# Optimization experiments

Measured on AMD Instinct MI355X. Metric: run time of the kernel, lower is better.

The kernel has to match this reference:

```python
import jax, jax.numpy as jnp
import numpy as np

B, S, D, H = 4, 2048, 512, 8


def _ln(x, g, b, eps=1e-5):
    m = x.mean(-1, keepdims=True)
    v = ((x - m) ** 2).mean(-1, keepdims=True)
    return (x - m) / jnp.sqrt(v + eps) * g + b


def setup_inputs() -> dict:
    key = jax.random.key(0)
    ks = iter(jax.random.split(key, 32))
    n = lambda shape, s=0.02: jax.random.normal(next(ks), shape, jnp.float32) * s
    z = lambda *shape: jnp.zeros(shape, jnp.float32)
    o = lambda *shape: jnp.ones(shape, jnp.float32)
    return {
        "x": jax.random.normal(next(ks), (B, S, D), jnp.float32),
        "x_prev": jax.random.normal(next(ks), (B, S, D), jnp.float32),
        "mu": jnp.float32(0.5),
        "in_proj_w": n((3 * D, D)), "in_proj_b": z(3 * D),
        "out_w": n((D, D)), "out_b": z(D),
        "ln1_g": o(D), "ln1_b": z(D),
        "time_mod": jnp.full((D,), 0.5, jnp.float32),
        "sm_ln_g": o(D), "sm_ln_b": z(D),
        "wr_w": n((D, D)), "wr_b": z(D),
        "wv_w": n((D, D)), "wv_b": z(D),
        "sc_ln_g": o(D), "sc_ln_b": z(D),
        "ln2_g": o(D), "ln2_b": z(D),
        "w1": n((4 * D, D)), "b1": z(4 * D),
        "w2": n((D, 4 * D)), "b2": z(D),
        "ln3_g": o(D), "ln3_b": z(D),
    }


def reference(x, x_prev, mu, in_proj_w, in_proj_b, out_w, out_b, ln1_g, ln1_b,
              time_mod, sm_ln_g, sm_ln_b, wr_w, wr_b, wv_w, wv_b,
              sc_ln_g, sc_ln_b, ln2_g, ln2_b, w1, b1, w2, b2, ln3_g, ln3_b):
    Bs, Sl, Dm = x.shape
    hd = Dm // H
    # Shift (x_prev is not None)
    shifted = mu * x + (1.0 - mu) * x_prev
    # Multihead self-attention (eval mode; dropout = identity)
    qkv = shifted @ in_proj_w.T + in_proj_b
    q, k, v = jnp.split(qkv, 3, axis=-1)
    q = q.reshape(Bs, Sl, H, hd)
    k = k.reshape(Bs, Sl, H, hd)
    v = v.reshape(Bs, Sl, H, hd)
    scores = jnp.einsum('bqhd,bkhd->bhqk', q, k) / jnp.sqrt(jnp.float32(hd))
    attn = jax.nn.softmax(scores, axis=-1)
    ao = jnp.einsum('bhqk,bkhd->bqhd', attn, v).reshape(Bs, Sl, Dm)
    ao = ao @ out_w.T + out_b
    x1 = _ln(shifted + ao, ln1_g, ln1_b)
    # SequenceMergingSeq with C = V = W = x1: sequential decayed running sums
    def step(carry, xt):  # xt: [B, D]
        a, b = carry
        decay = jax.nn.sigmoid(xt * time_mod)
        e = jnp.exp(xt)
        a = decay.mean(-1, keepdims=True) * a + e.sum(-1, keepdims=True)
        b = decay * b + e * xt
        return (a, b), b / (a + 1e-8)
    a0 = jnp.zeros((Bs, 1), x1.dtype)
    b0 = jnp.zeros((Bs, Dm), x1.dtype)
    _, outs = jax.lax.scan(step, (a0, b0), jnp.swapaxes(x1, 0, 1))  # [S,B,D]
    merged = _ln(jnp.swapaxes(outs, 0, 1), sm_ln_g, sm_ln_b)
    # StateCoupling
    coupled = _ln(jax.nn.sigmoid(merged @ wr_w.T + wr_b) * (merged @ wv_w.T + wv_b),
                  sc_ln_g, sc_ln_b)
    x2 = _ln(x1 + coupled, ln2_g, ln2_b)
    # FFN
    ffn = jax.nn.relu(x2 @ w1.T + b1) @ w2.T + b2
    return _ln(x2 + ffn, ln3_g, ln3_b)
```

## Files before the change

### kernel.cpp

```cpp
#include <hip/hip_runtime.h>
#include <math.h>

#define D_MODEL 512
#define SEQ     2048
#define BATCH   4
#define NH      8
#define HD      64
#define CHUNK   32
#define NCHUNK  64
#define M_TOK   (BATCH*SEQ)

typedef __attribute__((ext_vector_type(8))) short bhalf8;
typedef __attribute__((ext_vector_type(4))) float f32x4;

__device__ __forceinline__ float sigmoidf_(float x){ return 1.f/(1.f+expf(-x)); }

__device__ __forceinline__ unsigned short f2b(float f){
  unsigned u = __float_as_uint(f);
  u += 0x7FFFu + ((u>>16)&1u);
  return (unsigned short)(u>>16);
}
__device__ __forceinline__ float b2f(unsigned short h){
  return __uint_as_float(((unsigned)h)<<16);
}
__device__ __forceinline__ float blo(unsigned v){ return __uint_as_float(v<<16); }
__device__ __forceinline__ float bhi(unsigned v){ return __uint_as_float(v & 0xFFFF0000u); }
__device__ __forceinline__ unsigned bpack(float a, float b){
  return (unsigned)f2b(a) | ((unsigned)f2b(b)<<16);
}

__device__ __forceinline__ void gll16(const void* g, void* l){
  __builtin_amdgcn_global_load_lds(
      (const __attribute__((address_space(1))) unsigned int*)g,
      (__attribute__((address_space(3))) unsigned int*)l, 16, 0, 0);
}

__device__ __forceinline__ float exp2_hw(float x){
  float r;
  asm volatile("v_exp_f32 %0, %1" : "=v"(r) : "v"(x));
  return r;
}

__device__ __forceinline__ void block_sum2(float& a, float& b, float* lds){
  #pragma unroll
  for (int o=32;o>0;o>>=1){ a += __shfl_xor(a,o); b += __shfl_xor(b,o); }
  int w = threadIdx.x>>6, l = threadIdx.x&63;
  if (l==0){ lds[2*w]=a; lds[2*w+1]=b; }
  __syncthreads();
  float ta=0.f, tb=0.f; int nw = blockDim.x>>6;
  for (int i=0;i<nw;++i){ ta+=lds[2*i]; tb+=lds[2*i+1]; }
  a=ta; b=tb;
  __syncthreads();
}

__global__ void cvtshift_k(const float* __restrict__ s0,const float* __restrict__ s1,
                           const float* __restrict__ s2,const float* __restrict__ s3,
                           const float* __restrict__ s4,const float* __restrict__ s5,
                           unsigned short* __restrict__ d0,unsigned short* __restrict__ d1,
                           unsigned short* __restrict__ d2,unsigned short* __restrict__ d3,
                           unsigned short* __restrict__ d4,unsigned short* __restrict__ d5,
                           const float* __restrict__ x, const float* __restrict__ xp,
                           const float* __restrict__ mu,
                           unsigned short* __restrict__ ob){
  int t = blockIdx.x*blockDim.x + threadIdx.x;
  if (t < 917504){
    int j = t;
    const float* s; unsigned short* d;
    if (j < 196608){ s=s0; d=d0; }
    else if ((j-=196608) < 65536){ s=s1; d=d1; }
    else if ((j-=65536)  < 65536){ s=s2; d=d2; }
    else if ((j-=65536)  < 65536){ s=s3; d=d3; }
    else if ((j-=65536)  < 262144){ s=s4; d=d4; }
    else { j-=262144; s=s5; d=d5; }
    float4 v = ((const float4*)s)[j];
    uint2 p; p.x = bpack(v.x, v.y); p.y = bpack(v.z, v.w);
    ((uint2*)d)[j] = p;
  } else {
    int i = t - 917504;
    float m = mu[0];
    float4 a = ((const float4*)x)[i], p = ((const float4*)xp)[i];
    float4 r;
    r.x = m*a.x + (1.f-m)*p.x; r.y = m*a.y + (1.f-m)*p.y;
    r.z = m*a.z + (1.f-m)*p.z; r.w = m*a.w + (1.f-m)*p.w;
    uint2 q; q.x = bpack(r.x, r.y); q.y = bpack(r.z, r.w);
    ((uint2*)ob)[i] = q;
  }
}

template<int ACT, int OUTB>
__global__ __launch_bounds__(256) void mgemm_k(const unsigned short* __restrict__ A,
    const unsigned short* __restrict__ W, const float* __restrict__ bias,
    float* __restrict__ Yf, unsigned short* __restrict__ Yb, int Nd, int K){
  __shared__ unsigned short As[128*64];
  __shared__ unsigned short Bs[128*64];
  const int tid = threadIdx.x;
  const int w = tid>>6, lane = tid&63;
  const int l15 = lane&15, l4 = lane>>4;
  const int wr = w>>1, wc = w&1;
  const int nwg = gridDim.x*gridDim.y;
  const int orig = blockIdx.y*gridDim.x + blockIdx.x;
  const int swz = (orig&7)*(nwg>>3) + (orig>>3);
  const int bn = swz % gridDim.x;
  const int bm = swz / gridDim.x;

  const size_t Kb = (size_t)K*2;
  const int srow  = lane>>3;
  const int sbyte = ((lane&7)*16) ^ (srow<<4);
  const char* Ag = (const char*)A + (size_t)(bm*128)*Kb + sbyte;
  const char* Wg = (const char*)W + (size_t)(bn*128)*Kb + sbyte;

  f32x4 acc[4][4];
  const f32x4 z = {0.f,0.f,0.f,0.f};
  #pragma unroll
  for (int i=0;i<4;++i)
    #pragma unroll
    for (int j=0;j<4;++j) acc[i][j] = z;

  const int KT = K/64;
  for (int kt=0; kt<KT; ++kt){
    if (kt) __syncthreads();
    const size_t kOff = (size_t)kt*128;
    #pragma unroll
    for (int i=0;i<4;++i){
      int c = w*4 + i;
      int r = c*8 + srow;
      gll16(Ag + (size_t)r*Kb + kOff, (char*)As + c*1024);
      gll16(Wg + (size_t)r*Kb + kOff, (char*)Bs + c*1024);
    }
    __syncthreads();

    bhalf8 af[4][2], bf_[4][2];
    #pragma unroll
    for (int fr=0; fr<4; ++fr){
      int row = wr*64 + fr*16 + l15;
      #pragma unroll
      for (int ks=0; ks<2; ++ks){
        int byo = (l4*16 + ks*64) ^ ((row&7)<<4);
        af[fr][ks] = *(const bhalf8*)((const char*)As + row*128 + byo);
      }
    }
    #pragma unroll
    for (int fc=0; fc<4; ++fc){
      int row = wc*64 + fc*16 + l15;
      #pragma unroll
      for (int ks=0; ks<2; ++ks){
        int byo = (l4*16 + ks*64) ^ ((row&7)<<4);
        bf_[fc][ks] = *(const bhalf8*)((const char*)Bs + row*128 + byo);
      }
    }
    #pragma unroll
    for (int ks=0; ks<2; ++ks)
      #pragma unroll
      for (int fr=0; fr<4; ++fr)
        #pragma unroll
        for (int fc=0; fc<4; ++fc)
          acc[fr][fc] = __builtin_amdgcn_mfma_f32_16x16x32_bf16(af[fr][ks], bf_[fc][ks], acc[fr][fc], 0, 0, 0);
  }

  const int rowBase = bm*128 + wr*64;
  const int colBase = bn*128 + wc*64;
  #pragma unroll
  for (int fc=0; fc<4; ++fc){
    int col = colBase + fc*16 + l15;
    float bv = bias[col];
    #pragma unroll
    for (int fr=0; fr<4; ++fr){
      #pragma unroll
      for (int j=0; j<4; ++j){
        int row = rowBase + fr*16 + l4*4 + j;
        float v = acc[fr][fc][j] + bv;
        if (ACT) v = fmaxf(v, 0.f);
        if (OUTB) Yb[(size_t)row*Nd + col] = f2b(v);
        else      Yf[(size_t)row*Nd + col] = v;
      }
    }
  }
}

template<int ACT, int FUSE2, int SPLITK>
__global__ __launch_bounds__(256) void mgemm64_k(const unsigned short* __restrict__ A,
    const unsigned short* __restrict__ W0, const unsigned short* __restrict__ W1v,
    const float* __restrict__ bias0, const float* __restrict__ bias1,
    unsigned short* __restrict__ Yb0, unsigned short* __restrict__ Yb1,
    int Nd, int K){
  __shared__ unsigned short As[128*64];
  __shared__ unsigned short Bs[64*64];
  const int tid = threadIdx.x;
  const int w = tid>>6, lane = tid&63;
  const int l15 = lane&15, l4 = lane>>4;
  const int wr = w>>1, wc = w&1;
  const int nwg = gridDim.x*gridDim.y;
  const int orig = blockIdx.y*gridDim.x + blockIdx.x;
  const int swz = (orig&7)*(nwg>>3) + (orig>>3);
  int bn = swz % gridDim.x;
  const int bm = swz / gridDim.x;
  const unsigned short* W = W0;
  const float* bias = bias0;
  unsigned short* Yb = Yb0;
  int half = 0;
  if (FUSE2 && bn >= 8){ W = W1v; bias = bias1; Yb = Yb1; bn -= 8; }
  if (SPLITK && bn >= 8){ half = 1; Yb = Yb1; bn -= 8; }

  const int Ksr = SPLITK ? (K>>1) : K;
  const size_t Kb = (size_t)K*2;
  const size_t hOff = (size_t)half * Ksr * 2;
  const int srow  = lane>>3;
  const int sbyte = ((lane&7)*16) ^ (srow<<4);
  const char* Ag = (const char*)A + (size_t)(bm*128)*Kb + hOff + sbyte;
  const char* Wg = (const char*)W + (size_t)(bn*64)*Kb + hOff + sbyte;

  f32x4 acc[4][2];
  const f32x4 z = {0.f,0.f,0.f,0.f};
  #pragma unroll
  for (int i=0;i<4;++i)
    #pragma unroll
    for (int j=0;j<2;++j) acc[i][j] = z;

  const int KT = Ksr/64;
  for (int kt=0; kt<KT; ++kt){
    if (kt) __syncthreads();
    const size_t kOff = (size_t)kt*128;
    #pragma unroll
    for (int i=0;i<4;++i){
      int c = w*4 + i;
      int r = c*8 + srow;
      gll16(Ag + (size_t)r*Kb + kOff, (char*)As + c*1024);
    }
    #pragma unroll
    for (int i=0;i<2;++i){
      int c = w*2 + i;
      int r = c*8 + srow;
      gll16(Wg + (size_t)r*Kb + kOff, (char*)Bs + c*1024);
    }
    __syncthreads();

    bhalf8 af[4][2], bf_[2][2];
    #pragma unroll
    for (int fr=0; fr<4; ++fr){
      int row = wr*64 + fr*16 + l15;
      #pragma unroll
      for (int ks=0; ks<2; ++ks){
        int byo = (l4*16 + ks*64) ^ ((row&7)<<4);
        af[fr][ks] = *(const bhalf8*)((const char*)As + row*128 + byo);
      }
    }
    #pragma unroll
    for (int fc=0; fc<2; ++fc){
      int row = wc*32 + fc*16 + l15;
      #pragma unroll
      for (int ks=0; ks<2; ++ks){
        int byo = (l4*16 + ks*64) ^ ((row&7)<<4);
        bf_[fc][ks] = *(const bhalf8*)((const char*)Bs + row*128 + byo);
      }
    }
    #pragma unroll
    for (int ks=0; ks<2; ++ks)
      #pragma unroll
      for (int fr=0; fr<4; ++fr)
        #pragma unroll
        for (int fc=0; fc<2; ++fc)
          acc[fr][fc] = __builtin_amdgcn_mfma_f32_16x16x32_bf16(af[fr][ks], bf_[fc][ks], acc[fr][fc], 0, 0, 0);
  }

  const int rowBase = bm*128 + wr*64;
  const int colBase = bn*64 + wc*32;
  #pragma unroll
  for (int fc=0; fc<2; ++fc){
    int col = colBase + fc*16 + l15;
    float bv = (SPLITK && half) ? 0.f : bias[col];
    #pragma unroll
    for (int fr=0; fr<4; ++fr){
      #pragma unroll
      for (int j=0; j<4; ++j){
        int row = rowBase + fr*16 + l4*4 + j;
        float v = acc[fr][fc][j] + bv;
        if (ACT) v = fmaxf(v, 0.f);
        Yb[(size_t)row*Nd + col] = f2b(v);
      }
    }
  }
}

__global__ __launch_bounds__(512, 4) void fattn_k(const unsigned short* __restrict__ qkv,
                                                  unsigned short* __restrict__ ao){
  __shared__ unsigned short Ks[2][64*64];
  __shared__ unsigned short Vt[2][64*64];
  __shared__ unsigned short Ps[128*64];
  const int nwg = gridDim.x*gridDim.y*gridDim.z;
  const int orig = (blockIdx.z*gridDim.y + blockIdx.y)*gridDim.x + blockIdx.x;
  const int swz = (orig&7)*(nwg>>3) + (orig>>3);
  const int qt = swz % gridDim.x;
  const int rem = swz / gridDim.x;
  const int h = rem % gridDim.y;
  const int b = rem / gridDim.y;
  const int tid = threadIdx.x, w = tid>>6, lane = tid&63;
  const int l15 = lane&15, l4 = lane>>4;
  const size_t rowB = 3072;
  const char* base = (const char*)qkv + (size_t)b*SEQ*rowB;
  const char* Kg = base + 1024 + h*128;
  const char* Vg = base + 2048 + h*128;
  const float C2 = 0.18033688f;

  bhalf8 qf[2];
  {
    const char* qrow = base + (size_t)(qt*128 + w*16 + l15)*rowB + h*128;
    qf[0] = *(const bhalf8*)(qrow + l4*16);
    qf[1] = *(const bhalf8*)(qrow + l4*16 + 64);
  }
  bhalf8 v1;
  {
    short o = (l15==0) ? (short)0x3F80 : (short)0;
    v1 = (bhalf8){o,o,o,o,o,o,o,o};
  }

  const f32x4 z = {0.f,0.f,0.f,0.f};
  f32x4 oa[4], ol = z;
  #pragma unroll
  for (int i=0;i<4;++i) oa[i] = z;
  float mj = -INFINITY;

  const int srow  = lane>>3;
  const int sbyte = ((lane&7)*16) ^ (srow<<4);
  const int vd = lane;
  const int vsel = (vd>>3)&1;

  unsigned short vload[8];
  {
    int r = w*8 + srow;
    gll16(Kg + (size_t)r*rowB + sbyte, (char*)Ks[0] + w*1024);
  }
  #pragma unroll
  for (int i=0;i<8;++i)
    vload[i] = *(const unsigned short*)(Vg + (size_t)(w*8 + i)*rowB + vd*2);

  int cur = 0;
  for (int kt=0; kt<SEQ/64; ++kt){
    #pragma unroll
    for (int i=0;i<2;++i){
      int p = i ^ vsel;
      unsigned lo = (unsigned)vload[p*4+0] | ((unsigned)vload[p*4+1]<<16);
      unsigned hi = (unsigned)vload[p*4+2] | ((unsigned)vload[p*4+3]<<16);
      uint2 pk; pk.x = lo; pk.y = hi;
      int byo = (w*16 + p*8) ^ ((vd&7)<<4);
      *(uint2*)((char*)Vt[cur] + vd*128 + byo) = pk;
    }
    __syncthreads();

    if (kt+1 < SEQ/64){
      int r = w*8 + srow;
      gll16(Kg + (size_t)((kt+1)*64 + r)*rowB + sbyte, (char*)Ks[cur^1] + w*1024);
      #pragma unroll
      for (int i=0;i<8;++i)
        vload[i] = *(const unsigned short*)(Vg + (size_t)((kt+1)*64 + w*8 + i)*rowB + vd*2);
    }

    bhalf8 kf[4][2];
    #pragma unroll
    for (int fc=0; fc<4; ++fc){
      int kr = fc*16 + l15;
      #pragma unroll
      for (int ks=0; ks<2; ++ks){
        int byo = (l4*16 + ks*64) ^ ((kr&7)<<4);
        kf[fc][ks] = *(const bhalf8*)((const char*)Ks[cur] + kr*128 + byo);
      }
    }
    f32x4 s[4];
    #pragma unroll
    for (int i=0;i<4;++i) s[i] = z;
    __builtin_amdgcn_s_setprio(1);
    #pragma unroll
    for (int ks=0; ks<2; ++ks)
      #pragma unroll
      for (int fc=0; fc<4; ++fc)
        s[fc] = __builtin_amdgcn_mfma_f32_16x16x32_bf16(kf[fc][ks], qf[ks], s[fc], 0, 0, 0);
    __builtin_amdgcn_s_setprio(0);

    {
      float rm0 = fmaxf(fmaxf(s[0][0],s[0][1]), fmaxf(s[0][2],s[0][3]));
      float rm1 = fmaxf(fmaxf(s[1][0],s[1][1]), fmaxf(s[1][2],s[1][3]));
      float rm2 = fmaxf(fmaxf(s[2][0],s[2][1]), fmaxf(s[2][2],s[2][3]));
      float rm3 = fmaxf(fmaxf(s[3][0],s[3][1]), fmaxf(s[3][2],s[3][3]));
      float rm = fmaxf(fmaxf(rm0,rm1), fmaxf(rm2,rm3));
      rm = fmaxf(rm, __shfl_xor(rm,16));
      rm = fmaxf(rm, __shfl_xor(rm,32));
      float tmax = rm * C2;
      if (__any(tmax > mj + 8.f)){
        float mn = fmaxf(mj, tmax);
        float sc = exp2_hw(mj - mn);
        mj = mn;
        float scj0 = __shfl(sc, l4*4+0), scj1 = __shfl(sc, l4*4+1);
        float scj2 = __shfl(sc, l4*4+2), scj3 = __shfl(sc, l4*4+3);
        #pragma unroll
        for (int fc=0; fc<4; ++fc){
          oa[fc][0] *= scj0; oa[fc][1] *= scj1;
          oa[fc][2] *= scj2; oa[fc][3] *= scj3;
        }
        ol[0] *= scj0; ol[1] *= scj1; ol[2] *= scj2; ol[3] *= scj3;
      }
      int qrow = w*16 + l15;
      #pragma unroll
      for (int fc=0; fc<4; ++fc){
        float p0 = exp2_hw(fmaf(C2, s[fc][0], -mj));
        float p1 = exp2_hw(fmaf(C2, s[fc][1], -mj));
        float p2 = exp2_hw(fmaf(C2, s[fc][2], -mj));
        float p3 = exp2_hw(fmaf(C2, s[fc][3], -mj));
        unsigned lo, hi;
        asm volatile("v_cvt_pk_bf16_f32 %0, %1, %2" : "=v"(lo) : "v"(p0), "v"(p1));
        asm volatile("v_cvt_pk_bf16_f32 %0, %1, %2" : "=v"(hi) : "v"(p2), "v"(p3));
        uint2 pk; pk.x = lo; pk.y = hi;
        int byo = (fc*32 + l4*8) ^ ((l15&7)<<4);
        *(uint2*)((char*)Ps + qrow*128 + byo) = pk;
      }
    }

    bhalf8 vf[4][2];
    #pragma unroll
    for (int fc=0; fc<4; ++fc){
      int d = fc*16 + l15;
      #pragma unroll
      for (int ks=0; ks<2; ++ks){
        int byo = (ks*64 + l4*16) ^ ((d&7)<<4);
        vf[fc][ks] = *(const bhalf8*)((const char*)Vt[cur] + d*128 + byo);
      }
    }
    {
      int qrow = w*16 + l15;
      bhalf8 pf[2];
      #pragma unroll
      for (int ks=0; ks<2; ++ks){
        int byo = (ks*64 + l4*16) ^ ((l15&7)<<4);
        pf[ks] = *(const bhalf8*)((const char*)Ps + qrow*128 + byo);
      }
      __builtin_amdgcn_s_setprio(1);
      #pragma unroll
      for (int ks=0; ks<2; ++ks){
        #pragma unroll
        for (int fc=0; fc<4; ++fc)
          oa[fc] = __builtin_amdgcn_mfma_f32_16x16x32_bf16(pf[ks], vf[fc][ks], oa[fc], 0, 0, 0);
        ol = __builtin_amdgcn_mfma_f32_16x16x32_bf16(pf[ks], v1, ol, 0, 0, 0);
      }
      __builtin_amdgcn_s_setprio(0);
    }
    cur ^= 1;
  }

  {
    float li[4];
    #pragma unroll
    for (int j=0;j<4;++j) li[j] = 1.f/__shfl(ol[j], l4<<4);
    #pragma unroll
    for (int fc=0; fc<4; ++fc){
      int col = h*64 + fc*16 + l15;
      size_t r0 = (size_t)(b*SEQ + qt*128 + w*16 + l4*4);
      ao[(r0+0)*D_MODEL + col] = f2b(oa[fc][0]*li[0]);
      ao[(r0+1)*D_MODEL + col] = f2b(oa[fc][1]*li[1]);
      ao[(r0+2)*D_MODEL + col] = f2b(oa[fc][2]*li[2]);
      ao[(r0+3)*D_MODEL + col] = f2b(oa[fc][3]*li[3]);
    }
  }
}

__global__ __launch_bounds__(256) void lnfin_k(const unsigned int* __restrict__ X2b,
    const unsigned int* __restrict__ F0, const unsigned int* __restrict__ F1,
    const float* __restrict__ g, const float* __restrict__ be, float* __restrict__ outf){
  __shared__ float lds[16];
  const size_t off2 = (size_t)blockIdx.x * 256;
  const int tid = threadIdx.x;
  unsigned xv = X2b[off2+tid], f0 = F0[off2+tid], f1 = F1[off2+tid];
  float a0 = blo(xv) + blo(f0) + blo(f1);
  float a1 = bhi(xv) + bhi(f0) + bhi(f1);
  float s1 = a0+a1, s2 = a0*a0+a1*a1;
  block_sum2(s1, s2, lds);
  float mean = s1 * (1.f/512.f);
  float var  = s2 * (1.f/512.f) - mean*mean;
  float rstd = rsqrtf(var + 1e-5f);
  float2 gg = ((const float2*)g)[tid], bb = ((const float2*)be)[tid];
  float2 r;
  r.x = (a0-mean)*rstd*gg.x + bb.x;
  r.y = (a1-mean)*rstd*gg.y + bb.y;
  ((float2*)outf)[off2+tid] = r;
}

__global__ __launch_bounds__(256) void ln_scan_k(const unsigned int* __restrict__ Ab,
    const unsigned int* __restrict__ P0, const unsigned int* __restrict__ P1,
    const float* __restrict__ g, const float* __restrict__ be, const float* __restrict__ tm,
    unsigned int* __restrict__ x1b, unsigned int* __restrict__ dec, unsigned int* __restrict__ u,
    float* __restrict__ dm, float* __restrict__ es){
  __shared__ float lds[16];
  const size_t row = blockIdx.x;
  const size_t off2 = row * 256;
  const int tid = threadIdx.x;
  unsigned av = Ab[off2+tid], pv = P0[off2+tid], qv = P1[off2+tid];
  float a0 = blo(av) + blo(pv) + blo(qv);
  float a1 = bhi(av) + bhi(pv) + bhi(qv);
  float s1 = a0+a1, s2 = a0*a0+a1*a1;
  block_sum2(s1, s2, lds);
  float mean = s1 * (1.f/512.f);
  float var  = s2 * (1.f/512.f) - mean*mean;
  float rstd = rsqrtf(var + 1e-5f);
  float2 gg = ((const float2*)g)[tid], bb = ((const float2*)be)[tid], tt = ((const float2*)tm)[tid];
  float r0 = (a0-mean)*rstd*gg.x + bb.x;
  float r1 = (a1-mean)*rstd*gg.y + bb.y;
  x1b[off2+tid] = bpack(r0, r1);
  float dc0 = sigmoidf_(r0*tt.x), dc1 = sigmoidf_(r1*tt.y);
  float e0 = expf(r0), e1 = expf(r1);
  dec[off2+tid] = bpack(dc0, dc1);
  u[off2+tid]   = bpack(e0*r0, e1*r1);
  float dsum = dc0+dc1, esum = e0+e1;
  block_sum2(dsum, esum, lds);
  if (tid==0){ dm[row]=dsum*(1.f/512.f); es[row]=esum; }
}

__global__ __launch_bounds__(256) void ln2x_k(const unsigned int* __restrict__ R,
    const unsigned int* __restrict__ V, const unsigned int* __restrict__ X1,
    const float* __restrict__ g1, const float* __restrict__ b1_,
    const float* __restrict__ g2, const float* __restrict__ b2_,
    unsigned int* __restrict__ x2b){
  __shared__ float lds[16];
  const size_t off2 = (size_t)blockIdx.x * 256;
  const int tid = threadIdx.x;
  unsigned rv = R[off2+tid], vv = V[off2+tid];
  float a0 = sigmoidf_(blo(rv))*blo(vv);
  float a1 = sigmoidf_(bhi(rv))*bhi(vv);
  float s1 = a0+a1, s2 = a0*a0+a1*a1;
  block_sum2(s1, s2, lds);
  float mean = s1*(1.f/512.f);
  float var  = s2*(1.f/512.f) - mean*mean;
  float rstd = rsqrtf(var + 1e-5f);
  float2 g1v = ((const float2*)g1)[tid], b1v = ((const float2*)b1_)[tid];
  float c0 = (a0-mean)*rstd*g1v.x + b1v.x;
  float c1 = (a1-mean)*rstd*g1v.y + b1v.y;
  unsigned x1v = X1[off2+tid];
  float t0 = blo(x1v) + c0, t1 = bhi(x1v) + c1;
  float u1 = t0+t1, u2 = t0*t0+t1*t1;
  block_sum2(u1, u2, lds);
  float mean2 = u1*(1.f/512.f);
  float var2  = u2*(1.f/512.f) - mean2*mean2;
  float rstd2 = rsqrtf(var2 + 1e-5f);
  float2 g2v = ((const float2*)g2)[tid], b2v = ((const float2*)b2_)[tid];
  float r0 = (t0-mean2)*rstd2*g2v.x + b2v.x;
  float r1 = (t1-mean2)*rstd2*g2v.y + b2v.y;
  x2b[off2+tid] = bpack(r0, r1);
}

__global__ __launch_bounds__(256) void bscan_p1(const unsigned int* __restrict__ decay,
    const unsigned int* __restrict__ u, float* __restrict__ Gc, float* __restrict__ Uc){
  const int c = blockIdx.x, b = blockIdx.y, t = threadIdx.x;
  size_t base2 = ((size_t)b*SEQ + (size_t)c*CHUNK)*256 + t;
  float G0=1.f, G1=1.f, U0=0.f, U1=0.f;
  for (int i=0;i<CHUNK;++i){
    unsigned dv = decay[base2 + (size_t)i*256];
    unsigned uv = u[base2 + (size_t)i*256];
    float g0 = blo(dv), g1 = bhi(dv);
    U0 = g0*U0 + blo(uv); G0 *= g0;
    U1 = g1*U1 + bhi(uv); G1 *= g1;
  }
  size_t idx2 = ((size_t)b*NCHUNK + c)*256 + t;
  float2 gv; gv.x=G0; gv.y=G1;
  float2 uv2; uv2.x=U0; uv2.y=U1;
  ((float2*)Gc)[idx2] = gv;
  ((float2*)Uc)[idx2] = uv2;
}

__global__ __launch_bounds__(512) void scan2_k(const float* __restrict__ Gc, const float* __restrict__ Uc,
    float* __restrict__ binit, const float* __restrict__ dm, const float* __restrict__ es,
    float* __restrict__ a_out){
  __shared__ float sG[512], sU[512];
  if (blockIdx.x < 4){
    const int b = blockIdx.x, d = threadIdx.x;
    float cur = 0.f;
    for (int c0=0; c0<NCHUNK; c0+=8){
      float g[8], u[8];
      #pragma unroll
      for (int i=0;i<8;++i){
        size_t idx = ((size_t)b*NCHUNK + c0+i)*D_MODEL + d;
        g[i] = Gc[idx]; u[i] = Uc[idx];
      }
      #pragma unroll
      for (int i=0;i<8;++i){
        size_t idx = ((size_t)b*NCHUNK + c0+i)*D_MODEL + d;
        binit[idx] = cur;
        cur = g[i]*cur + u[i];
      }
    }
  } else {
    const int b = blockIdx.x - 4, tid = threadIdx.x;
    const float* dmb = dm + (size_t)b*SEQ;
    const float* esb = es + (size_t)b*SEQ;
    const int t0 = tid*4;
    float gi[4], ui[4];
    #pragma unroll
    for (int i=0;i<4;++i){ gi[i]=dmb[t0+i]; ui[i]=esb[t0+i]; }
    float G=1.f, U=0.f;
    #pragma unroll
    for (int i=0;i<4;++i){ U = gi[i]*U + ui[i]; G *= gi[i]; }
    sG[tid]=G; sU[tid]=U;
    __syncthreads();
    for (int off=1; off<512; off<<=1){
      float pg=1.f, pu=0.f;
      bool act = tid >= off;
      if (act){ pg = sG[tid-off]; pu = sU[tid-off]; }
      __syncthreads();
      if (act){ sU[tid] = sG[tid]*pu + sU[tid]; sG[tid] = sG[tid]*pg; }
      __syncthreads();
    }
    float a = (tid==0) ? 0.f : sU[tid-1];
    #pragma unroll
    for (int i=0;i<4;++i){ a = gi[i]*a + ui[i]; a_out[(size_t)b*SEQ + t0 + i] = a; }
  }
}

__global__ __launch_bounds__(256) void p3ln_k(const unsigned int* __restrict__ decay,
    const unsigned int* __restrict__ u,
    const float* __restrict__ binit, const float* __restrict__ a,
    const float* __restrict__ g, const float* __restrict__ be,
    unsigned int* __restrict__ mb){
  __shared__ float lds[16];
  const int c = blockIdx.x, b = blockIdx.y, t = threadIdx.x;
  size_t base2 = ((size_t)b*SEQ + (size_t)c*CHUNK)*256 + t;
  float2 bv = ((const float2*)binit)[((size_t)b*NCHUNK + c)*256 + t];
  float2 gg = ((const float2*)g)[t], bb = ((const float2*)be)[t];
  for (int i=0;i<CHUNK;++i){
    unsigned dv = decay[base2 + (size_t)i*256];
    unsigned uv = u[base2 + (size_t)i*256];
    bv.x = blo(dv)*bv.x + blo(uv);
    bv.y = bhi(dv)*bv.y + bhi(uv);
    float av = a[(size_t)b*SEQ + (size_t)c*CHUNK + i];
    float inv = 1.f/(av + 1e-8f);
    float v0 = bv.x*inv, v1 = bv.y*inv;
    float s1 = v0+v1, s2 = v0*v0+v1*v1;
    block_sum2(s1, s2, lds);
    float mean = s1*(1.f/512.f);
    float var  = s2*(1.f/512.f) - mean*mean;
    float rstd = rsqrtf(var + 1e-5f);
    mb[base2 + (size_t)i*256] = bpack((v0-mean)*rstd*gg.x + bb.x,
                                      (v1-mean)*rstd*gg.y + bb.y);
  }
}

extern "C" void kernel_launch(void* const* d_in, const int* in_sizes, int n_in,
                              void* d_out, int out_size, void* d_ws, size_t ws_size,
                              hipStream_t stream){
  const float* x     = (const float*)d_in[0];
  const float* xp    = (const float*)d_in[1];
  const float* mu    = (const float*)d_in[2];
  const float* in_w  = (const float*)d_in[3];
  const float* in_b  = (const float*)d_in[4];
  const float* out_w = (const float*)d_in[5];
  const float* out_b = (const float*)d_in[6];
  const float* ln1_g = (const float*)d_in[7];
  const float* ln1_b = (const float*)d_in[8];
  const float* tm    = (const float*)d_in[9];
  const float* sm_g  = (const float*)d_in[10];
  const float* sm_b  = (const float*)d_in[11];
  const float* wr_w  = (const float*)d_in[12];
  const float* wr_b  = (const float*)d_in[13];
  const float* wv_w  = (const float*)d_in[14];
  const float* wv_b  = (const float*)d_in[15];
  const float* sc_g  = (const float*)d_in[16];
  const float* sc_b  = (const float*)d_in[17];
  const float* ln2_g = (const float*)d_in[18];
  const float* ln2_b = (const float*)d_in[19];
  const float* w1    = (const float*)d_in[20];
  const float* b1    = (const float*)d_in[21];
  const float* w2    = (const float*)d_in[22];
  const float* b2    = (const float*)d_in[23];
  const float* ln3_g = (const float*)d_in[24];
  const float* ln3_b = (const float*)d_in[25];
  float* out = (float*)d_out;
  float* ws  = (float*)d_ws;

  const size_t N = (size_t)M_TOK*D_MODEL;
  unsigned short* P0b = (unsigned short*)ws;
  unsigned short* X1b = (unsigned short*)ws + N;
  unsigned short* F0  = (unsigned short*)(ws + N);
  unsigned short* F1  = (unsigned short*)(ws + N) + N;
  unsigned short* P1b = (unsigned short*)(ws + 2*N);
  float* EX  = ws + 3*N;
  float* dm    = EX;
  float* es    = EX + 8192;
  float* aarr  = EX + 16384;
  float* Gc    = EX + 24576;
  float* Uc    = Gc + 131072;
  float* binit = Uc + 131072;

  unsigned short* SB = (unsigned short*)(ws + 3*N + N/4);
  unsigned short* Wq = SB;
  unsigned short* Wo = Wq + 786432;
  unsigned short* Wr = Wo + 262144;
  unsigned short* Wv = Wr + 262144;
  unsigned short* W1 = Wv + 262144;
  unsigned short* W2 = W1 + 1048576;
  unsigned short* Xb = W2 + 1048576;
  unsigned short* Mb = Xb + N;
  unsigned short* U  = Mb + N;
  unsigned short* Qb  = U;
  unsigned short* AOb = U + 12*1024*1024;
  unsigned short* ub   = U;
  unsigned short* decb = U + 12*1024*1024;
  unsigned short* Rb   = U;
  unsigned short* Vb   = U + 4*1024*1024;
  unsigned short* Hb   = U;

  cvtshift_k<<<7680, 256, 0, stream>>>(in_w, out_w, wr_w, wv_w, w1, w2,
                                       Wq, Wo, Wr, Wv, W1, W2,
                                       x, xp, mu, Xb);
  mgemm_k<0,1><<<dim3(12,64), 256, 0, stream>>>(Xb, Wq, in_b, nullptr, Qb, 1536, 512);
  fattn_k<<<dim3(SEQ/128, NH, BATCH), 512, 0, stream>>>(Qb, AOb);
  mgemm64_k<0,0,1><<<dim3(16,64), 256, 0, stream>>>(AOb, Wo, nullptr, out_b, nullptr,
                                                    P0b, P1b, 512, 512);
  ln_scan_k<<<M_TOK, 256, 0, stream>>>((const unsigned int*)Xb, (const unsigned int*)P0b,
                                       (const unsigned int*)P1b,
                                       ln1_g, ln1_b, tm,
                                       (unsigned int*)X1b, (unsigned int*)decb, (unsigned int*)ub,
                                       dm, es);
  bscan_p1<<<dim3(NCHUNK, BATCH), 256, 0, stream>>>((const unsigned int*)decb, (const unsigned int*)ub, Gc, Uc);
  scan2_k<<<8, 512, 0, stream>>>(Gc, Uc, binit, dm, es, aarr);
  p3ln_k<<<dim3(NCHUNK, BATCH), 256, 0, stream>>>((const unsigned int*)decb, (const unsigned int*)ub,
                                                  binit, aarr, sm_g, sm_b, (unsigned int*)Mb);
  mgemm64_k<0,1,0><<<dim3(16,64), 256, 0, stream>>>(Mb, Wr, Wv, wr_b, wv_b,
                                                    Rb, Vb, 512, 512);
  ln2x_k<<<M_TOK, 256, 0, stream>>>((const unsigned int*)Rb, (const unsigned int*)Vb,
                                    (const unsigned int*)X1b,
                                    sc_g, sc_b, ln2_g, ln2_b, (unsigned int*)Xb);
  mgemm_k<1,1><<<dim3(16,64), 256, 0, stream>>>(Xb, W1, b1, nullptr, Hb, 2048, 512);
  mgemm64_k<0,0,1><<<dim3(16,64), 256, 0, stream>>>(Hb, W2, nullptr, b2, nullptr,
                                                    F0, F1, 512, 2048);
  lnfin_k<<<M_TOK, 256, 0, stream>>>((const unsigned int*)Xb, (const unsigned int*)F0,
                                     (const unsigned int*)F1, ln3_g, ln3_b, out);
}
```

Before: 251.0 us.

## Use one wavefront per row in LayerNorm kernels with 16-byte vector loads

Each LayerNorm-style kernel (ln_scan, ln2x, lnfin, p3ln) now gives one 64-lane wavefront a 512-element row, with each lane handling 8 bf16 values through uint4 loads and stores. The block-wide reduction through LDS and two __syncthreads is replaced by a pure shuffle reduction within the wave. This removes barrier and LDS traffic and cuts the number of memory instructions. p3ln runs with 64-thread blocks, so only 256 single-wave blocks drive the chunked scan, which may underfill the GPU.

New measurement: 237.9 us. -5.2%, faster.

```diff
diff --git a/kernel.cpp b/kernel.cpp
--- a/kernel.cpp
+++ b/kernel.cpp
@@ -41,16 +41,9 @@
   return r;
 }
 
-__device__ __forceinline__ void block_sum2(float& a, float& b, float* lds){
+__device__ __forceinline__ void wave_red2(float& a, float& b){
   #pragma unroll
   for (int o=32;o>0;o>>=1){ a += __shfl_xor(a,o); b += __shfl_xor(b,o); }
-  int w = threadIdx.x>>6, l = threadIdx.x&63;
-  if (l==0){ lds[2*w]=a; lds[2*w+1]=b; }
-  __syncthreads();
-  float ta=0.f, tb=0.f; int nw = blockDim.x>>6;
-  for (int i=0;i<nw;++i){ ta+=lds[2*i]; tb+=lds[2*i+1]; }
-  a=ta; b=tb;
-  __syncthreads();
 }
 
 __global__ void cvtshift_k(const float* __restrict__ s0,const float* __restrict__ s1,
@@ -460,87 +453,134 @@
   }
 }
 
-__global__ __launch_bounds__(256) void lnfin_k(const unsigned int* __restrict__ X2b,
-    const unsigned int* __restrict__ F0, const unsigned int* __restrict__ F1,
+__global__ __launch_bounds__(256) void lnfin_k(const uint4* __restrict__ X2b,
+    const uint4* __restrict__ F0, const uint4* __restrict__ F1,
     const float* __restrict__ g, const float* __restrict__ be, float* __restrict__ outf){
-  __shared__ float lds[16];
-  const size_t off2 = (size_t)blockIdx.x * 256;
-  const int tid = threadIdx.x;
-  unsigned xv = X2b[off2+tid], f0 = F0[off2+tid], f1 = F1[off2+tid];
-  float a0 = blo(xv) + blo(f0) + blo(f1);
-  float a1 = bhi(xv) + bhi(f0) + bhi(f1);
-  float s1 = a0+a1, s2 = a0*a0+a1*a1;
-  block_sum2(s1, s2, lds);
+  const int row = blockIdx.x*4 + (threadIdx.x>>6);
+  const int l = threadIdx.x & 63;
+  const size_t i4 = (size_t)row*64 + l;
+  uint4 xv = X2b[i4], f0 = F0[i4], f1 = F1[i4];
+  float a[8];
+  a[0]=blo(xv.x)+blo(f0.x)+blo(f1.x); a[1]=bhi(xv.x)+bhi(f0.x)+bhi(f1.x);
+  a[2]=blo(xv.y)+blo(f0.y)+blo(f1.y); a[3]=bhi(xv.y)+bhi(f0.y)+bhi(f1.y);
+  a[4]=blo(xv.z)+blo(f0.z)+blo(f1.z); a[5]=bhi(xv.z)+bhi(f0.z)+bhi(f1.z);
+  a[6]=blo(xv.w)+blo(f0.w)+blo(f1.w); a[7]=bhi(xv.w)+bhi(f0.w)+bhi(f1.w);
+  float s1=0.f, s2=0.f;
+  #pragma unroll
+  for (int k=0;k<8;++k){ s1 += a[k]; s2 += a[k]*a[k]; }
+  wave_red2(s1, s2);
   float mean = s1 * (1.f/512.f);
   float var  = s2 * (1.f/512.f) - mean*mean;
   float rstd = rsqrtf(var + 1e-5f);
-  float2 gg = ((const float2*)g)[tid], bb = ((const float2*)be)[tid];
-  float2 r;
-  r.x = (a0-mean)*rstd*gg.x + bb.x;
-  r.y = (a1-mean)*rstd*gg.y + bb.y;
-  ((float2*)outf)[off2+tid] = r;
-}
-
-__global__ __launch_bounds__(256) void ln_scan_k(const unsigned int* __restrict__ Ab,
-    const unsigned int* __restrict__ P0, const unsigned int* __restrict__ P1,
+  float4 g0 = ((const float4*)g)[l*2], g1 = ((const float4*)g)[l*2+1];
+  float4 b0 = ((const float4*)be)[l*2], b1 = ((const float4*)be)[l*2+1];
+  float4 r0, r1;
+  r0.x=(a[0]-mean)*rstd*g0.x+b0.x; r0.y=(a[1]-mean)*rstd*g0.y+b0.y;
+  r0.z=(a[2]-mean)*rstd*g0.z+b0.z; r0.w=(a[3]-mean)*rstd*g0.w+b0.w;
+  r1.x=(a[4]-mean)*rstd*g1.x+b1.x; r1.y=(a[5]-mean)*rstd*g1.y+b1.y;
+  r1.z=(a[6]-mean)*rstd*g1.z+b1.z; r1.w=(a[7]-mean)*rstd*g1.w+b1.w;
+  ((float4*)outf)[(size_t)row*128 + l*2]     = r0;
+  ((float4*)outf)[(size_t)row*128 + l*2 + 1] = r1;
+}
+
+__global__ __launch_bounds__(256) void ln_scan_k(const uint4* __restrict__ Ab,
+    const uint4* __restrict__ P0, const uint4* __restrict__ P1,
     const float* __restrict__ g, const float* __restrict__ be, const float* __restrict__ tm,
-    unsigned int* __restrict__ x1b, unsigned int* __restrict__ dec, unsigned int* __restrict__ u,
+    uint4* __restrict__ x1b, uint4* __restrict__ dec, uint4* __restrict__ u,
     float* __restrict__ dm, float* __restrict__ es){
-  __shared__ float lds[16];
-  const size_t row = blockIdx.x;
-  const size_t off2 = row * 256;
-  const int tid = threadIdx.x;
-  unsigned av = Ab[off2+tid], pv = P0[off2+tid], qv = P1[off2+tid];
-  float a0 = blo(av) + blo(pv) + blo(qv);
-  float a1 = bhi(av) + bhi(pv) + bhi(qv);
-  float s1 = a0+a1, s2 = a0*a0+a1*a1;
-  block_sum2(s1, s2, lds);
+  const int row = blockIdx.x*4 + (threadIdx.x>>6);
+  const int l = threadIdx.x & 63;
+  const size_t i4 = (size_t)row*64 + l;
+  uint4 av = Ab[i4], pv = P0[i4], qv = P1[i4];
+  float a[8];
+  a[0]=blo(av.x)+blo(pv.x)+blo(qv.x); a[1]=bhi(av.x)+bhi(pv.x)+bhi(qv.x);
+  a[2]=blo(av.y)+blo(pv.y)+blo(qv.y); a[3]=bhi(av.y)+bhi(pv.y)+bhi(qv.y);
+  a[4]=blo(av.z)+blo(pv.z)+blo(qv.z); a[5]=bhi(av.z)+bhi(pv.z)+bhi(qv.z);
+  a[6]=blo(av.w)+blo(pv.w)+blo(qv.w); a[7]=bhi(av.w)+bhi(pv.w)+bhi(qv.w);
+  float s1=0.f, s2=0.f;
+  #pragma unroll
+  for (int k=0;k<8;++k){ s1 += a[k]; s2 += a[k]*a[k]; }
+  wave_red2(s1, s2);
   float mean = s1 * (1.f/512.f);
   float var  = s2 * (1.f/512.f) - mean*mean;
   float rstd = rsqrtf(var + 1e-5f);
-  float2 gg = ((const float2*)g)[tid], bb = ((const float2*)be)[tid], tt = ((const float2*)tm)[tid];
-  float r0 = (a0-mean)*rstd*gg.x + bb.x;
-  float r1 = (a1-mean)*rstd*gg.y + bb.y;
-  x1b[off2+tid] = bpack(r0, r1);
-  float dc0 = sigmoidf_(r0*tt.x), dc1 = sigmoidf_(r1*tt.y);
-  float e0 = expf(r0), e1 = expf(r1);
-  dec[off2+tid] = bpack(dc0, dc1);
-  u[off2+tid]   = bpack(e0*r0, e1*r1);
-  float dsum = dc0+dc1, esum = e0+e1;
-  block_sum2(dsum, esum, lds);
-  if (tid==0){ dm[row]=dsum*(1.f/512.f); es[row]=esum; }
-}
-
-__global__ __launch_bounds__(256) void ln2x_k(const unsigned int* __restrict__ R,
-    const unsigned int* __restrict__ V, const unsigned int* __restrict__ X1,
+  float4 g0 = ((const float4*)g)[l*2], g1 = ((const float4*)g)[l*2+1];
+  float4 b0 = ((const float4*)be)[l*2], b1 = ((const float4*)be)[l*2+1];
+  float4 t0 = ((const float4*)tm)[l*2], t1 = ((const float4*)tm)[l*2+1];
+  float r[8];
+  r[0]=(a[0]-mean)*rstd*g0.x+b0.x; r[1]=(a[1]-mean)*rstd*g0.y+b0.y;
+  r[2]=(a[2]-mean)*rstd*g0.z+b0.z; r[3]=(a[3]-mean)*rstd*g0.w+b0.w;
+  r[4]=(a[4]-mean)*rstd*g1.x+b1.x; r[5]=(a[5]-mean)*rstd*g1.y+b1.y;
+  r[6]=(a[6]-mean)*rstd*g1.z+b1.z; r[7]=(a[7]-mean)*rstd*g1.w+b1.w;
+  uint4 xo; xo.x=bpack(r[0],r[1]); xo.y=bpack(r[2],r[3]); xo.z=bpack(r[4],r[5]); xo.w=bpack(r[6],r[7]);
+  x1b[i4] = xo;
+  float tmv[8] = {t0.x,t0.y,t0.z,t0.w,t1.x,t1.y,t1.z,t1.w};
+  float dc[8], e[8];
+  float dsum=0.f, esum=0.f;
+  #pragma unroll
+  for (int k=0;k<8;++k){
+    dc[k] = sigmoidf_(r[k]*tmv[k]);
+    e[k]  = expf(r[k]);
+    dsum += dc[k]; esum += e[k];
+  }
+  uint4 dv; dv.x=bpack(dc[0],dc[1]); dv.y=bpack(dc[2],dc[3]); dv.z=bpack(dc[4],dc[5]); dv.w=bpack(dc[6],dc[7]);
+  uint4 uv; uv.x=bpack(e[0]*r[0],e[1]*r[1]); uv.y=bpack(e[2]*r[2],e[3]*r[3]);
+  uv.z=bpack(e[4]*r[4],e[5]*r[5]); uv.w=bpack(e[6]*r[6],e[7]*r[7]);
+  dec[i4] = dv; u[i4] = uv;
+  wave_red2(dsum, esum);
+  if (l==0){ dm[row]=dsum*(1.f/512.f); es[row]=esum; }
+}
+
+__global__ __launch_bounds__(256) void ln2x_k(const uint4* __restrict__ R,
+    const uint4* __restrict__ V, const uint4* __restrict__ X1,
     const float* __restrict__ g1, const float* __restrict__ b1_,
     const float* __restrict__ g2, const float* __restrict__ b2_,
-    unsigned int* __restrict__ x2b){
-  __shared__ float lds[16];
-  const size_t off2 = (size_t)blockIdx.x * 256;
-  const int tid = threadIdx.x;
-  unsigned rv = R[off2+tid], vv = V[off2+tid];
-  float a0 = sigmoidf_(blo(rv))*blo(vv);
-  float a1 = sigmoidf_(bhi(rv))*bhi(vv);
-  float s1 = a0+a1, s2 = a0*a0+a1*a1;
-  block_sum2(s1, s2, lds);
+    uint4* __restrict__ x2b){
+  const int row = blockIdx.x*4 + (threadIdx.x>>6);
+  const int l = threadIdx.x & 63;
+  const size_t i4 = (size_t)row*64 + l;
+  uint4 rv = R[i4], vv = V[i4];
+  float a[8];
+  a[0]=sigmoidf_(blo(rv.x))*blo(vv.x); a[1]=sigmoidf_(bhi(rv.x))*bhi(vv.x);
+  a[2]=sigmoidf_(blo(rv.y))*blo(vv.y); a[3]=sigmoidf_(bhi(rv.y))*bhi(vv.y);
+  a[4]=sigmoidf_(blo(rv.z))*blo(vv.z); a[5]=sigmoidf_(bhi(rv.z))*bhi(vv.z);
+  a[6]=sigmoidf_(blo(rv.w))*blo(vv.w); a[7]=sigmoidf_(bhi(rv.w))*bhi(vv.w);
+  float s1=0.f, s2=0.f;
+  #pragma unroll
+  for (int k=0;k<8;++k){ s1 += a[k]; s2 += a[k]*a[k]; }
+  wave_red2(s1, s2);
   float mean = s1*(1.f/512.f);
   float var  = s2*(1.f/512.f) - mean*mean;
   float rstd = rsqrtf(var + 1e-5f);
-  float2 g1v = ((const float2*)g1)[tid], b1v = ((const float2*)b1_)[tid];
-  float c0 = (a0-mean)*rstd*g1v.x + b1v.x;
-  float c1 = (a1-mean)*rstd*g1v.y + b1v.y;
-  unsigned x1v = X1[off2+tid];
-  float t0 = blo(x1v) + c0, t1 = bhi(x1v) + c1;
-  float u1 = t0+t1, u2 = t0*t0+t1*t1;
-  block_sum2(u1, u2, lds);
+  float4 g10 = ((const float4*)g1)[l*2], g11 = ((const float4*)g1)[l*2+1];
+  float4 b10 = ((const float4*)b1_)[l*2], b11 = ((const float4*)b1_)[l*2+1];
+  float c[8];
+  c[0]=(a[0]-mean)*rstd*g10.x+b10.x; c[1]=(a[1]-mean)*rstd*g10.y+b10.y;
+  c[2]=(a[2]-mean)*rstd*g10.z+b10.z; c[3]=(a[3]-mean)*rstd*g10.w+b10.w;
+  c[4]=(a[4]-mean)*rstd*g11.x+b11.x; c[5]=(a[5]-mean)*rstd*g11.y+b11.y;
+  c[6]=(a[6]-mean)*rstd*g11.z+b11.z; c[7]=(a[7]-mean)*rstd*g11.w+b11.w;
+  uint4 x1v = X1[i4];
+  float t[8];
+  t[0]=blo(x1v.x)+c[0]; t[1]=bhi(x1v.x)+c[1];
+  t[2]=blo(x1v.y)+c[2]; t[3]=bhi(x1v.y)+c[3];
+  t[4]=blo(x1v.z)+c[4]; t[5]=bhi(x1v.z)+c[5];
+  t[6]=blo(x1v.w)+c[6]; t[7]=bhi(x1v.w)+c[7];
+  float u1=0.f, u2=0.f;
+  #pragma unroll
+  for (int k=0;k<8;++k){ u1 += t[k]; u2 += t[k]*t[k]; }
+  wave_red2(u1, u2);
   float mean2 = u1*(1.f/512.f);
   float var2  = u2*(1.f/512.f) - mean2*mean2;
   float rstd2 = rsqrtf(var2 + 1e-5f);
-  float2 g2v = ((const float2*)g2)[tid], b2v = ((const float2*)b2_)[tid];
-  float r0 = (t0-mean2)*rstd2*g2v.x + b2v.x;
-  float r1 = (t1-mean2)*rstd2*g2v.y + b2v.y;
-  x2b[off2+tid] = bpack(r0, r1);
+  float4 g20 = ((const float4*)g2)[l*2], g21 = ((const float4*)g2)[l*2+1];
+  float4 b20 = ((const float4*)b2_)[l*2], b21 = ((const float4*)b2_)[l*2+1];
+  float o[8];
+  o[0]=(t[0]-mean2)*rstd2*g20.x+b20.x; o[1]=(t[1]-mean2)*rstd2*g20.y+b20.y;
+  o[2]=(t[2]-mean2)*rstd2*g20.z+b20.z; o[3]=(t[3]-mean2)*rstd2*g20.w+b20.w;
+  o[4]=(t[4]-mean2)*rstd2*g21.x+b21.x; o[5]=(t[5]-mean2)*rstd2*g21.y+b21.y;
+  o[6]=(t[6]-mean2)*rstd2*g21.z+b21.z; o[7]=(t[7]-mean2)*rstd2*g21.w+b21.w;
+  uint4 xo; xo.x=bpack(o[0],o[1]); xo.y=bpack(o[2],o[3]); xo.z=bpack(o[4],o[5]); xo.w=bpack(o[6],o[7]);
+  x2b[i4] = xo;
 }
 
 __global__ __launch_bounds__(256) void bscan_p1(const unsigned int* __restrict__ decay,
@@ -610,31 +650,45 @@
   }
 }
 
-__global__ __launch_bounds__(256) void p3ln_k(const unsigned int* __restrict__ decay,
-    const unsigned int* __restrict__ u,
+__global__ __launch_bounds__(64) void p3ln_k(const uint4* __restrict__ decay,
+    const uint4* __restrict__ u,
     const float* __restrict__ binit, const float* __restrict__ a,
     const float* __restrict__ g, const float* __restrict__ be,
-    unsigned int* __restrict__ mb){
-  __shared__ float lds[16];
-  const int c = blockIdx.x, b = blockIdx.y, t = threadIdx.x;
-  size_t base2 = ((size_t)b*SEQ + (size_t)c*CHUNK)*256 + t;
-  float2 bv = ((const float2*)binit)[((size_t)b*NCHUNK + c)*256 + t];
-  float2 gg = ((const float2*)g)[t], bb = ((const float2*)be)[t];
+    uint4* __restrict__ mb){
+  const int c = blockIdx.x, b = blockIdx.y, l = threadIdx.x;
+  const size_t rowBase = (size_t)b*SEQ + (size_t)c*CHUNK;
+  float4 bv0 = ((const float4*)binit)[((size_t)b*NCHUNK + c)*128 + l*2];
+  float4 bv1 = ((const float4*)binit)[((size_t)b*NCHUNK + c)*128 + l*2 + 1];
+  float bv[8] = {bv0.x,bv0.y,bv0.z,bv0.w,bv1.x,bv1.y,bv1.z,bv1.w};
+  float4 g0 = ((const float4*)g)[l*2], g1 = ((const float4*)g)[l*2+1];
+  float4 b0 = ((const float4*)be)[l*2], b1 = ((const float4*)be)[l*2+1];
+  float gv[8] = {g0.x,g0.y,g0.z,g0.w,g1.x,g1.y,g1.z,g1.w};
+  float bb[8] = {b0.x,b0.y,b0.z,b0.w,b1.x,b1.y,b1.z,b1.w};
   for (int i=0;i<CHUNK;++i){
-    unsigned dv = decay[base2 + (size_t)i*256];
-    unsigned uv = u[base2 + (size_t)i*256];
-    bv.x = blo(dv)*bv.x + blo(uv);
-    bv.y = bhi(dv)*bv.y + bhi(uv);
-    float av = a[(size_t)b*SEQ + (size_t)c*CHUNK + i];
+    size_t i4 = (rowBase + i)*64 + l;
+    uint4 dv = decay[i4], uv = u[i4];
+    float dc[8] = {blo(dv.x),bhi(dv.x),blo(dv.y),bhi(dv.y),blo(dv.z),bhi(dv.z),blo(dv.w),bhi(dv.w)};
+    float uu[8] = {blo(uv.x),bhi(uv.x),blo(uv.y),bhi(uv.y),blo(uv.z),bhi(uv.z),blo(uv.w),bhi(uv.w)};
+    float val[8];
+    float av = a[rowBase + i];
     float inv = 1.f/(av + 1e-8f);
-    float v0 = bv.x*inv, v1 = bv.y*inv;
-    float s1 = v0+v1, s2 = v0*v0+v1*v1;
-    block_sum2(s1, s2, lds);
+    float s1=0.f, s2=0.f;
+    #pragma unroll
+    for (int k=0;k<8;++k){
+      bv[k] = dc[k]*bv[k] + uu[k];
+      val[k] = bv[k]*inv;
+      s1 += val[k]; s2 += val[k]*val[k];
+    }
+    wave_red2(s1, s2);
     float mean = s1*(1.f/512.f);
     float var  = s2*(1.f/512.f) - mean*mean;
     float rstd = rsqrtf(var + 1e-5f);
-    mb[base2 + (size_t)i*256] = bpack((v0-mean)*rstd*gg.x + bb.x,
-                                      (v1-mean)*rstd*gg.y + bb.y);
+    uint4 mo;
+    mo.x = bpack((val[0]-mean)*rstd*gv[0]+bb[0], (val[1]-mean)*rstd*gv[1]+bb[1]);
+    mo.y = bpack((val[2]-mean)*rstd*gv[2]+bb[2], (val[3]-mean)*rstd*gv[3]+bb[3]);
+    mo.z = bpack((val[4]-mean)*rstd*gv[4]+bb[4], (val[5]-mean)*rstd*gv[5]+bb[5]);
+    mo.w = bpack((val[6]-mean)*rstd*gv[6]+bb[6], (val[7]-mean)*rstd*gv[7]+bb[7]);
+    mb[i4] = mo;
   }
 }
 
@@ -709,23 +763,23 @@
   fattn_k<<<dim3(SEQ/128, NH, BATCH), 512, 0, stream>>>(Qb, AOb);
   mgemm64_k<0,0,1><<<dim3(16,64), 256, 0, stream>>>(AOb, Wo, nullptr, out_b, nullptr,
                                                     P0b, P1b, 512, 512);
-  ln_scan_k<<<M_TOK, 256, 0, stream>>>((const unsigned int*)Xb, (const unsigned int*)P0b,
-                                       (const unsigned int*)P1b,
-                                       ln1_g, ln1_b, tm,
-                                       (unsigned int*)X1b, (unsigned int*)decb, (unsigned int*)ub,
-                                       dm, es);
+  ln_scan_k<<<M_TOK/4, 256, 0, stream>>>((const uint4*)Xb, (const uint4*)P0b,
+                                         (const uint4*)P1b,
+                                         ln1_g, ln1_b, tm,
+                                         (uint4*)X1b, (uint4*)decb, (uint4*)ub,
+                                         dm, es);
   bscan_p1<<<dim3(NCHUNK, BATCH), 256, 0, stream>>>((const unsigned int*)decb, (const unsigned int*)ub, Gc, Uc);
   scan2_k<<<8, 512, 0, stream>>>(Gc, Uc, binit, dm, es, aarr);
-  p3ln_k<<<dim3(NCHUNK, BATCH), 256, 0, stream>>>((const unsigned int*)decb, (const unsigned int*)ub,
-                                                  binit, aarr, sm_g, sm_b, (unsigned int*)Mb);
+  p3ln_k<<<dim3(NCHUNK, BATCH), 64, 0, stream>>>((const uint4*)decb, (const uint4*)ub,
+                                                 binit, aarr, sm_g, sm_b, (uint4*)Mb);
   mgemm64_k<0,1,0><<<dim3(16,64), 256, 0, stream>>>(Mb, Wr, Wv, wr_b, wv_b,
                                                     Rb, Vb, 512, 512);
-  ln2x_k<<<M_TOK, 256, 0, stream>>>((const unsigned int*)Rb, (const unsigned int*)Vb,
-                                    (const unsigned int*)X1b,
-                                    sc_g, sc_b, ln2_g, ln2_b, (unsigned int*)Xb);
+  ln2x_k<<<M_TOK/4, 256, 0, stream>>>((const uint4*)Rb, (const uint4*)Vb,
+                                      (const uint4*)X1b,
+                                      sc_g, sc_b, ln2_g, ln2_b, (uint4*)Xb);
   mgemm_k<1,1><<<dim3(16,64), 256, 0, stream>>>(Xb, W1, b1, nullptr, Hb, 2048, 512);
   mgemm64_k<0,0,1><<<dim3(16,64), 256, 0, stream>>>(Hb, W2, nullptr, b2, nullptr,
                                                     F0, F1, 512, 2048);
-  lnfin_k<<<M_TOK, 256, 0, stream>>>((const unsigned int*)Xb, (const unsigned int*)F0,
-                                     (const unsigned int*)F1, ln3_g, ln3_b, out);
-}
+  lnfin_k<<<M_TOK/4, 256, 0, stream>>>((const uint4*)Xb, (const uint4*)F0,
+                                       (const uint4*)F1, ln3_g, ln3_b, out);
+}
```
